# Kernel tuning notes

Hardware: AMD Instinct MI355X
Metric: run time of the kernel (lower is better)

## Reference

```python
import jax, jax.numpy as jnp
import numpy as np

STEP_SIZE = 0.1
FLOW_STRENGTH = 5.0
MAX_STEPS = 16  # points in [0,1)^2 -> max dist sqrt(2) -> at most floor(14.14)+1 = 15 steps
NNODES = 1024


def setup_inputs() -> dict:
    key = jax.random.key(0)
    ks = jax.random.split(key, 7)
    def lin(k, fan_in, shape):
        bound = 1.0 / np.sqrt(fan_in)
        return jax.random.uniform(k, shape, jnp.float32, -bound, bound)
    return {
        "embedded_points": jax.random.uniform(ks[0], (NNODES, 2), jnp.float32),
        "W1": lin(ks[1], 2, (2, 10)),  "b1": lin(ks[2], 2, (10,)),
        "W2": lin(ks[3], 10, (10, 10)), "b2": lin(ks[4], 10, (10,)),
        "W3": lin(ks[5], 10, (10, 2)),  "b3": lin(ks[6], 10, (2,)),
    }


def _flowfield(x, W1, b1, W2, b2, W3, b3):
    h = jnp.tanh(x @ W1 + b1)
    h = jnp.tanh(h @ W2 + b2)
    return h @ W3 + b3


def reference(embedded_points, W1, b1, W2, b2, W3, b3):
    # Pairwise path-integral cost matrix embedding_D[i, j] = cost(x_i, x_j)
    x1 = embedded_points[:, None, :]            # [n,1,2]
    x2 = embedded_points[None, :, :]            # [1,n,2]
    delta = x2 - x1                              # [n,n,2]
    euc = jnp.linalg.norm(delta, axis=-1)        # [n,n]
    safe_euc = jnp.where(euc > 0, euc, 1.0)
    unit = delta / safe_euc[..., None]           # [n,n,2]

    t = jnp.arange(MAX_STEPS, dtype=embedded_points.dtype)   # [S]
    # steps_to_x2: x1 + t * step_size * (x2-x1)/||x2-x1||   -> [n,n,S,2]
    steps = x1[:, :, None, :] + (t[:, None] * STEP_SIZE) * unit[:, :, None, :]

    flow = _flowfield(steps, W1, b1, W2, b2, W3, b3)          # [n,n,S,2]
    dot = jnp.einsum("ijsd,ijd->ijs", flow, delta)            # [n,n,S]
    e = jnp.exp(dot)
    cost_normalizer = FLOW_STRENGTH * e / (FLOW_STRENGTH - 1.0 + e)
    per_step = STEP_SIZE / cost_normalizer                    # [n,n,S]

    # original loops t in range(int(euc/step_size)+1): valid iff t <= floor(euc/step_size)
    n_valid = jnp.floor(euc / STEP_SIZE)                      # [n,n]
    valid = t[None, None, :] <= n_valid[..., None]            # [n,n,S]
    cost = jnp.sum(jnp.where(valid, per_step, 0.0), axis=-1)  # [n,n]
    # torch.allclose(x1, x2) -> cost 0 (identical points)
    return jnp.where(euc > 0, cost, 0.0)
```

## Files before the change

### kernel.cpp

```cpp
#include <hip/hip_runtime.h>
#include <hip/hip_fp16.h>

typedef float v2 __attribute__((ext_vector_type(2)));

constexpr int NN = 1024;
constexpr int GC = 64;
constexpr float GS = 64.0f;
constexpr int NC = GC * GC;

__device__ __forceinline__ float fast_tanh(float x) {
    float e = exp2f(x * 2.88539008177792681472f);
    return 1.0f - 2.0f * __builtin_amdgcn_rcpf(1.0f + e);
}

__device__ __forceinline__ v2 mlp_eval(float x, float y,
    const float* __restrict__ W1, const float* __restrict__ b1,
    const float* __restrict__ W2, const float* __restrict__ b2,
    const float* __restrict__ W3, const float* __restrict__ b3)
{
    float h1[10], h2[10];
#pragma unroll
    for (int k = 0; k < 10; ++k)
        h1[k] = fast_tanh(fmaf(x, W1[k], fmaf(y, W1[10 + k], b1[k])));
#pragma unroll
    for (int k = 0; k < 10; ++k) {
        float acc = b2[k];
#pragma unroll
        for (int l = 0; l < 10; ++l) acc = fmaf(h1[l], W2[10 * l + k], acc);
        h2[k] = fast_tanh(acc);
    }
    float f0 = b3[0], f1 = b3[1];
#pragma unroll
    for (int k = 0; k < 10; ++k) {
        f0 = fmaf(h2[k], W3[2 * k], f0);
        f1 = fmaf(h2[k], W3[2 * k + 1], f1);
    }
    v2 r; r.x = f0; r.y = f1;
    return r;
}

__device__ __forceinline__ unsigned pack2h(float lo, float hi) {
    return (unsigned)__half_as_ushort(__float2half(lo))
         | ((unsigned)__half_as_ushort(__float2half(hi)) << 16);
}

__device__ __forceinline__ float2 unpack2h(unsigned u) {
    union { unsigned x; __half2 h; } c; c.x = u;
    return __half22float2(c.h);
}

__global__ __launch_bounds__(256) void cells_kernel(
    const float* __restrict__ W1, const float* __restrict__ b1,
    const float* __restrict__ W2, const float* __restrict__ b2,
    const float* __restrict__ W3, const float* __restrict__ b3,
    uint4* __restrict__ g)
{
    const int c = blockIdx.x * 256 + threadIdx.x;
    if (c >= NC) return;
    const int ix = c & (GC - 1), iy = c >> 6;
    const float x0 = (float)ix * (1.0f / GS), x1 = (float)(ix + 1) * (1.0f / GS);
    const float y0 = (float)iy * (1.0f / GS), y1 = (float)(iy + 1) * (1.0f / GS);

    const v2 f00 = mlp_eval(x0, y0, W1, b1, W2, b2, W3, b3);
    const v2 f10 = mlp_eval(x1, y0, W1, b1, W2, b2, W3, b3);
    const v2 f01 = mlp_eval(x0, y1, W1, b1, W2, b2, W3, b3);

    uint4 w;
    w.x = pack2h(f00.x, f00.y);
    w.y = pack2h(f10.x - f00.x, f10.y - f00.y);
    w.z = pack2h(f01.x - f00.x, f01.y - f00.y);
    w.w = 0;
    g[c] = w;
}

__global__ __launch_bounds__(1024, 8) void flow_kernel(
    const float* __restrict__ pts,
    const uint4* __restrict__ g,
    float* __restrict__ out)
{
    __shared__ uint4 tabL[NC];

    const int t = threadIdx.x;
#pragma unroll
    for (int k = 0; k < 4; ++k)
        tabL[t + 1024 * k] = g[t + 1024 * k];
    __syncthreads();

    const v2 pj = ((const v2*)pts)[t];
    const float x2x = pj.x, x2y = pj.y;

#pragma unroll 1
    for (int q = 0; q < 2; ++q) {
        const int i = (blockIdx.x << 1) + q;
        const float x1x = pts[2 * i], x1y = pts[2 * i + 1];
        const float dx = x2x - x1x, dy = x2y - x1y;

        const float nrm2 = __fadd_rn(__fmul_rn(dx, dx), __fmul_rn(dy, dy));
        const float euc  = __fsqrt_rn(nrm2);
        const float se   = (euc > 0.0f) ? euc : 1.0f;
        const float ux   = __fdiv_rn(dx, se), uy = __fdiv_rn(dy, se);
        const int   nvi  = (int)floorf(__fdiv_rn(euc, 0.1f));
        const int   smax = (nvi < 15) ? nvi : 15;

        float pu = x1x * GS, pv = x1y * GS;
        const float du = 6.4f * ux, dv = 6.4f * uy;
        const float dxe = -1.44269504088896340736f * dx;
        const float dye = -1.44269504088896340736f * dy;

        float cost = 0.0f;
#pragma unroll 1
        for (int s = 0; s <= smax; ++s) {
            int ix = (int)pu; ix = (ix < GC - 1) ? ix : (GC - 1);
            int iy = (int)pv; iy = (iy < GC - 1) ? iy : (GC - 1);
            const float tx = pu - (float)ix;
            const float ty = pv - (float)iy;

            const uint4 w = tabL[(iy << 6) + ix];
            const float2 a   = unpack2h(w.x);
            const float2 gdx = unpack2h(w.y);
            const float2 gdy = unpack2h(w.z);
            const float fx = fmaf(ty, gdy.x, fmaf(tx, gdx.x, a.x));
            const float fy = fmaf(ty, gdy.y, fmaf(tx, gdx.y, a.y));

            const float de = fmaf(fx, dxe, fy * dye);
            cost += fmaf(0.08f, exp2f(de), 0.02f);

            pu += du; pv += dv;
        }

        out[(i << 10) | t] = (euc > 0.0f) ? cost : 0.0f;
    }
}

extern "C" void kernel_launch(void* const* d_in, const int* in_sizes, int n_in,
                              void* d_out, int out_size, void* d_ws, size_t ws_size,
                              hipStream_t stream) {
    const float* pts = (const float*)d_in[0];
    const float* W1  = (const float*)d_in[1];
    const float* b1  = (const float*)d_in[2];
    const float* W2  = (const float*)d_in[3];
    const float* b2  = (const float*)d_in[4];
    const float* W3  = (const float*)d_in[5];
    const float* b3  = (const float*)d_in[6];
    float* out = (float*)d_out;

    uint4* g = (uint4*)d_ws;

    cells_kernel<<<NC / 256, 256, 0, stream>>>(W1, b1, W2, b2, W3, b3, g);
    flow_kernel<<<NN / 2, 1024, 0, stream>>>(pts, g, out);
}
```

Baseline: 22.27 us.

## Sort pair work by step count within block to reduce wavefront divergence

Each block counting-sorts its 2048 (i,j) pairs by loop trip count, using ballots, a shared-memory prefix scan and a permutation table. Wavefronts then process pairs with similar step counts, and short and long buckets are paired across the two rounds, so lanes are not left idle waiting on the longest path. This adds sort overhead, extra barriers and scattered output writes. It also shrinks the cells_kernel blocks to 64 threads and unrolls the step loop by 2.

```diff
diff --git a/kernel.cpp b/kernel.cpp
--- a/kernel.cpp
+++ b/kernel.cpp
@@ -49,13 +49,13 @@
     return __half22float2(c.h);
 }
 
-__global__ __launch_bounds__(256) void cells_kernel(
+__global__ __launch_bounds__(64) void cells_kernel(
     const float* __restrict__ W1, const float* __restrict__ b1,
     const float* __restrict__ W2, const float* __restrict__ b2,
     const float* __restrict__ W3, const float* __restrict__ b3,
     uint4* __restrict__ g)
 {
-    const int c = blockIdx.x * 256 + threadIdx.x;
+    const int c = blockIdx.x * 64 + threadIdx.x;
     if (c >= NC) return;
     const int ix = c & (GC - 1), iy = c >> 6;
     const float x0 = (float)ix * (1.0f / GS), x1 = (float)(ix + 1) * (1.0f / GS);
@@ -79,20 +79,75 @@
     float* __restrict__ out)
 {
     __shared__ uint4 tabL[NC];
+    __shared__ v2 ptsL[NN];
+    __shared__ unsigned short ordQ[2 * NN];
 
     const int t = threadIdx.x;
+    const int lane = t & 63, w = t >> 6;
+    const int i0 = blockIdx.x << 1;
+
+    ptsL[t] = ((const v2*)pts)[t];
+    __syncthreads();
+
+    int key[2];
+#pragma unroll
+    for (int q = 0; q < 2; ++q) {
+        const int i = i0 + q;
+        const float ddx = ptsL[t].x - ptsL[i].x;
+        const float ddy = ptsL[t].y - ptsL[i].y;
+        const float n2 = __fadd_rn(__fmul_rn(ddx, ddx), __fmul_rn(ddy, ddy));
+        const float e  = __fsqrt_rn(n2);
+        const int  nv  = (int)floorf(__fdiv_rn(e, 0.1f));
+        key[q] = (nv < 15) ? nv : 15;
+    }
+
+    int* cntA = (int*)tabL;
+    int* cntB = (int*)tabL + 512;
+    const unsigned long long lt = (lane == 0) ? 0ull : (~0ull >> (64 - lane));
+    int myRank[2];
+#pragma unroll
+    for (int q = 0; q < 2; ++q) {
+#pragma unroll
+        for (int k = 0; k < 16; ++k) {
+            const unsigned long long m = __ballot(key[q] == k);
+            if (key[q] == k) myRank[q] = __popcll(m & lt);
+            if (lane == k) cntA[(k << 5) | (w << 1) | q] = __popcll(m);
+        }
+    }
+    __syncthreads();
+
+    int orig = 0;
+    if (t < 512) orig = cntA[t];
+    int* src = cntA; int* dst = cntB;
+    for (int off = 1; off < 512; off <<= 1) {
+        if (t < 512) { int x = src[t]; if (t >= off) x += src[t - off]; dst[t] = x; }
+        __syncthreads();
+        int* tmp = src; src = dst; dst = tmp;
+    }
+    if (t < 512) dst[t] = src[t] - orig;
+    __syncthreads();
+
+#pragma unroll
+    for (int q = 0; q < 2; ++q) {
+        const int slot = dst[(key[q] << 5) | (w << 1) | q] + myRank[q];
+        ordQ[slot] = (unsigned short)((q << 10) | t);
+    }
+    __syncthreads();
+
 #pragma unroll
     for (int k = 0; k < 4; ++k)
         tabL[t + 1024 * k] = g[t + 1024 * k];
     __syncthreads();
 
-    const v2 pj = ((const v2*)pts)[t];
-    const float x2x = pj.x, x2y = pj.y;
-
 #pragma unroll 1
-    for (int q = 0; q < 2; ++q) {
-        const int i = (blockIdx.x << 1) + q;
-        const float x1x = pts[2 * i], x1y = pts[2 * i + 1];
+    for (int r = 0; r < 2; ++r) {
+        const int sidx = (r == 0) ? w : (31 - w);
+        const int item = ordQ[(sidx << 6) | lane];
+        const int q = item >> 10, jj = item & (NN - 1);
+        const int i = i0 + q;
+
+        const float x1x = ptsL[i].x,  x1y = ptsL[i].y;
+        const float x2x = ptsL[jj].x, x2y = ptsL[jj].y;
         const float dx = x2x - x1x, dy = x2y - x1y;
 
         const float nrm2 = __fadd_rn(__fmul_rn(dx, dx), __fmul_rn(dy, dy));
@@ -108,17 +163,17 @@
         const float dye = -1.44269504088896340736f * dy;
 
         float cost = 0.0f;
-#pragma unroll 1
+#pragma unroll 2
         for (int s = 0; s <= smax; ++s) {
             int ix = (int)pu; ix = (ix < GC - 1) ? ix : (GC - 1);
             int iy = (int)pv; iy = (iy < GC - 1) ? iy : (GC - 1);
             const float tx = pu - (float)ix;
             const float ty = pv - (float)iy;
 
-            const uint4 w = tabL[(iy << 6) + ix];
-            const float2 a   = unpack2h(w.x);
-            const float2 gdx = unpack2h(w.y);
-            const float2 gdy = unpack2h(w.z);
+            const uint4 cw = tabL[(iy << 6) + ix];
+            const float2 a   = unpack2h(cw.x);
+            const float2 gdx = unpack2h(cw.y);
+            const float2 gdy = unpack2h(cw.z);
             const float fx = fmaf(ty, gdy.x, fmaf(tx, gdx.x, a.x));
             const float fy = fmaf(ty, gdy.y, fmaf(tx, gdx.y, a.y));
 
@@ -128,7 +183,7 @@
             pu += du; pv += dv;
         }
 
-        out[(i << 10) | t] = (euc > 0.0f) ? cost : 0.0f;
+        out[(i << 10) | jj] = (euc > 0.0f) ? cost : 0.0f;
     }
 }
 
@@ -146,6 +201,6 @@
 
     uint4* g = (uint4*)d_ws;
 
-    cells_kernel<<<NC / 256, 256, 0, stream>>>(W1, b1, W2, b2, W3, b3, g);
+    cells_kernel<<<NC / 64, 64, 0, stream>>>(W1, b1, W2, b2, W3, b3, g);
     flow_kernel<<<NN / 2, 1024, 0, stream>>>(pts, g, out);
 }
```

New measurement: 25.52 us. 14.6% more time.
